# Performance work log

Hardware: AMD Instinct MI355X
Metric: run time of the kernel (lower is better)

The kernel has to match this reference:

```python
import jax, jax.numpy as jnp
import numpy as np

N_NODE = 4096        # graph size (dense adjacency is N_NODE x N_NODE)
N_EDGES = 131072     # avg degree 32
N_TARGETS = 512      # anomaly target list length (self.lst in original)
EPS = 1e-20


def setup_inputs() -> dict:
    key = jax.random.key(0)
    k1, k2, k3 = jax.random.split(key, 3)
    src = jax.random.randint(k1, (N_EDGES,), 0, N_NODE)
    dst = jax.random.randint(k2, (N_EDGES,), 0, N_NODE)
    tri_idx = jnp.stack([src, dst], axis=1).astype(jnp.int64)   # [m, 2] (src, dst)
    tri_w = jnp.ones((N_EDGES,), dtype=jnp.float32)             # [m] edge weights
    lst = jax.random.randint(k3, (N_TARGETS,), 0, N_NODE).astype(jnp.int64)
    return {"tri_idx": tri_idx, "tri_w": tri_w, "lst": lst}


def _forward(tri_idx, tri_w, lst):
    n = N_NODE
    # adjacency_matrix: scatter-add coo -> dense, then symmetrize minus diag
    A = jnp.zeros((n, n), dtype=tri_w.dtype).at[tri_idx[:, 0], tri_idx[:, 1]].add(tri_w)
    A = A + A.T - jnp.diag(jnp.diag(A))

    # extract_NE: N = row sums; E = row sums + 0.5 * diag(A^3)
    N = jnp.sum(A, axis=1)                      # [n]
    A2 = A @ A                                  # [n, n]
    diag_A3 = jnp.einsum('ik,ki->i', A2, A)     # diag(A @ A @ A) without full A^3
    E = N + 0.5 * diag_A3                       # [n]
    Ncol = N.reshape(-1, 1)                     # [n, 1]

    # OLS_estimation: theta = pinv([1, log N]) @ log E
    logN = jnp.log(Ncol + EPS)                  # [n, 1]
    logE = jnp.log(E + EPS)                     # [n]
    logN1 = jnp.concatenate([jnp.ones((n, 1), dtype=logN.dtype), logN], axis=1)  # [n, 2]
    theta = jnp.linalg.pinv(logN1) @ logE       # [2]
    b, w = theta[0], theta[1]

    # sum of squared power-law residuals over target list (vectorized loop)
    resid = jnp.exp(b) * N[lst] ** w - E[lst]   # [len(lst)]
    return jnp.sum(resid ** 2).reshape(1)       # original accumulates shape-[1] terms


def reference(tri_idx, tri_w, lst):
    return _forward(tri_idx, tri_w, lst)
```

## Files before the change

### kernel.cpp

```cpp
#include <hip/hip_runtime.h>
#include <math.h>

#define NN   4096
#define NN4  (NN/4)
#define CAP  128
#define RPB  2
#define D3B  (NN/RPB)
#define NGRP (D3B/64)
#define GPAD 32
#define CPAD 32

#define C_TGRP  0
#define C_TGLOB (32 * GPAD)

#define OFF_CNT  4608
#define OFF_ENTP 528896
#define OFF_ND   1577472
#define OFF_GSUM 1610240
#define ZBYTES   OFF_ND
#define Z4       (ZBYTES / 16)

__global__ __launch_bounds__(256) void zeroall_kernel(float4* __restrict__ z) {
    int t = blockIdx.x * 256 + threadIdx.x;
    if (t < Z4) z[t] = make_float4(0.f, 0.f, 0.f, 0.f);
}

__global__ void scatter_kernel(const int* __restrict__ idx,
                               const float* __restrict__ wgt,
                               int* __restrict__ cnt,
                               unsigned short* __restrict__ entp, int m) {
    int e = blockIdx.x * blockDim.x + threadIdx.x;
    if (e < m) {
        int2 sd = ((const int2*)idx)[e];
        int s = sd.x, d = sd.y;
        unsigned ival = (unsigned)(int)wgt[e];
        if (ival > 15u) ival = 15u;
        int p = atomicAdd(cnt + s * CPAD, 1);
        if (p < CAP) entp[(size_t)s * CAP + p] = (unsigned short)(((unsigned)d << 4) | ival);
        if (s != d) {
            int q = atomicAdd(cnt + d * CPAD, 1);
            if (q < CAP) entp[(size_t)d * CAP + q] = (unsigned short)(((unsigned)s << 4) | ival);
        }
    }
}

__global__ __launch_bounds__(256, 8) void diag3stats_kernel(
        const int* __restrict__ cnt, const unsigned* __restrict__ entp32,
        unsigned long long* __restrict__ ND,
        const int* __restrict__ lst, int nl,
        int* __restrict__ ctr, double* __restrict__ gsum,
        float* __restrict__ out) {
    __shared__ int    lrow[NN];
    __shared__ int    lcol[CAP];
    __shared__ int    lval[CAP];
    __shared__ int    redI[8];
    __shared__ int    flag;
    __shared__ double dsum[4][4];
    __shared__ double wb[2];
    __shared__ double sh[4];

    const int tid = threadIdx.x, bid = blockIdx.x;
    const int warp = tid >> 6, lane = tid & 63;
    const int i0 = bid * RPB;

    int mi_arr[RPB];
    #pragma unroll
    for (int r = 0; r < RPB; ++r) {
        int c = cnt[(i0 + r) * CPAD];
        mi_arr[r] = c > CAP ? CAP : c;
    }
    unsigned q_arr[RPB] = {0u, 0u};
    if (tid < 64) {
        #pragma unroll
        for (int r = 0; r < RPB; ++r)
            q_arr[r] = entp32[(size_t)(i0 + r) * 64 + tid];
    }

    int4* l4 = (int4*)lrow;
    for (int rr = 0; rr < RPB; ++rr) {
        const int i = i0 + rr;
        const int mi = mi_arr[rr];
        for (int k = tid; k < NN4; k += 256) l4[k] = make_int4(0, 0, 0, 0);
        __syncthreads();

        int nsum = 0;
        if (tid < 64) {
            unsigned q = q_arr[rr];
            unsigned e0 = q & 0xffffu, e1 = q >> 16;
            int c0 = (int)(e0 >> 4), c1 = (int)(e1 >> 4);
            int w0 = (int)(e0 & 15u), w1 = (int)(e1 & 15u);
            lcol[2 * tid]     = c0; lval[2 * tid]     = w0;
            lcol[2 * tid + 1] = c1; lval[2 * tid + 1] = w1;
            if (w0) atomicAdd(&lrow[c0], w0);
            if (w1) atomicAdd(&lrow[c1], w1);
            nsum = w0 + w1;
        }
        if (warp == 0) {
            for (int o = 32; o; o >>= 1) nsum += __shfl_down(nsum, o);
            if (lane == 0) redI[0] = nsum;
        }
        __syncthreads();

        int acc = 0;
        for (int t = warp; t < mi; t += 16) {
            const int t1 = t + 4, t2 = t + 8, t3 = t + 12;
            const bool b1 = t1 < mi, b2 = t2 < mi, b3 = t3 < mi;
            int c0 = lcol[t];
            int c1 = b1 ? lcol[t1] : 0;
            int c2 = b2 ? lcol[t2] : 0;
            int c3 = b3 ? lcol[t3] : 0;
            int a0 = lval[t];
            int a1 = b1 ? lval[t1] : 0;
            int a2 = b2 ? lval[t2] : 0;
            int a3 = b3 ? lval[t3] : 0;
            unsigned q0 = entp32[(size_t)c0 * 64 + lane];
            unsigned q1 = entp32[(size_t)c1 * 64 + lane];
            unsigned q2 = entp32[(size_t)c2 * 64 + lane];
            unsigned q3 = entp32[(size_t)c3 * 64 + lane];
            int d0 = (int)(q0 & 15u) * lrow[(q0 >> 4) & 4095u]
                   + (int)((q0 >> 16) & 15u) * lrow[q0 >> 20];
            int d1 = (int)(q1 & 15u) * lrow[(q1 >> 4) & 4095u]
                   + (int)((q1 >> 16) & 15u) * lrow[q1 >> 20];
            int d2 = (int)(q2 & 15u) * lrow[(q2 >> 4) & 4095u]
                   + (int)((q2 >> 16) & 15u) * lrow[q2 >> 20];
            int d3 = (int)(q3 & 15u) * lrow[(q3 >> 4) & 4095u]
                   + (int)((q3 >> 16) & 15u) * lrow[q3 >> 20];
            acc += a0 * d0 + a1 * d1 + a2 * d2 + a3 * d3;
        }
        for (int o = 32; o; o >>= 1) acc += __shfl_down(acc, o);
        if (lane == 0) redI[4 + warp] = acc;
        __syncthreads();

        if (tid == 0) {
            float2 nd = make_float2((float)redI[0],
                                    (float)(redI[4] + redI[5] + redI[6] + redI[7]));
            unsigned long long bits;
            __builtin_memcpy(&bits, &nd, 8);
            __hip_atomic_store(ND + i, bits, __ATOMIC_RELAXED, __HIP_MEMORY_SCOPE_AGENT);
        }
        __syncthreads();
    }

    if (tid == 0) {
        asm volatile("s_waitcnt vmcnt(0)" ::: "memory");
        int v = __hip_atomic_fetch_add(ctr + C_TGRP + (bid >> 6) * GPAD, 1,
                                       __ATOMIC_RELAXED, __HIP_MEMORY_SCOPE_AGENT);
        flag = (v == 63);
    }
    __syncthreads();
    if (!flag) return;

    const int g = bid >> 6;
    {
        double p1 = 0, p2 = 0, p3 = 0, p4 = 0;
        if (tid < 128) {
            unsigned long long bits = __hip_atomic_load(ND + (g * 128 + tid),
                                                        __ATOMIC_RELAXED, __HIP_MEMORY_SCOPE_AGENT);
            float2 nd; __builtin_memcpy(&nd, &bits, 8);
            double Nd = (double)nd.x;
            double Ed = Nd + 0.5 * (double)nd.y;
            double ln = (double)logf((float)(Nd + 1e-20));
            double le = (double)logf((float)(Ed + 1e-20));
            p1 = ln; p2 = ln * ln; p3 = le; p4 = ln * le;
        }
        for (int o = 32; o; o >>= 1) {
            p1 += __shfl_down(p1, o);
            p2 += __shfl_down(p2, o);
            p3 += __shfl_down(p3, o);
            p4 += __shfl_down(p4, o);
        }
        if (lane == 0) {
            dsum[warp][0] = p1; dsum[warp][1] = p2;
            dsum[warp][2] = p3; dsum[warp][3] = p4;
        }
        __syncthreads();
        if (tid == 0) {
            for (int k = 0; k < 4; ++k) {
                double v = dsum[0][k] + dsum[1][k] + dsum[2][k] + dsum[3][k];
                __hip_atomic_store(gsum + g * 4 + k, v, __ATOMIC_RELAXED,
                                   __HIP_MEMORY_SCOPE_AGENT);
            }
            asm volatile("s_waitcnt vmcnt(0)" ::: "memory");
            int vg = __hip_atomic_fetch_add(ctr + C_TGLOB, 1,
                                            __ATOMIC_RELAXED, __HIP_MEMORY_SCOPE_AGENT);
            flag = (vg == NGRP - 1);
        }
    }
    __syncthreads();
    if (!flag) return;

    if (warp == 0) {
        double s1 = 0, s2 = 0, t0 = 0, t1 = 0;
        if (lane < NGRP) {
            s1 = __hip_atomic_load(gsum + lane * 4 + 0, __ATOMIC_RELAXED, __HIP_MEMORY_SCOPE_AGENT);
            s2 = __hip_atomic_load(gsum + lane * 4 + 1, __ATOMIC_RELAXED, __HIP_MEMORY_SCOPE_AGENT);
            t0 = __hip_atomic_load(gsum + lane * 4 + 2, __ATOMIC_RELAXED, __HIP_MEMORY_SCOPE_AGENT);
            t1 = __hip_atomic_load(gsum + lane * 4 + 3, __ATOMIC_RELAXED, __HIP_MEMORY_SCOPE_AGENT);
        }
        for (int o = 32; o; o >>= 1) {
            s1 += __shfl_down(s1, o);
            s2 += __shfl_down(s2, o);
            t0 += __shfl_down(t0, o);
            t1 += __shfl_down(t1, o);
        }
        if (lane == 0) {
            double n = (double)NN;
            double det = n * s2 - s1 * s1;
            wb[0] = (n * t1 - s1 * t0) / det;
            wb[1] = (s2 * t0 - s1 * t1) / det;
        }
    }
    __syncthreads();
    const double w = wb[0];
    const double eb = exp(wb[1]);
    const float wf = (float)w;
    double racc = 0;
    for (int p = tid; p < nl; p += 256) {
        int r = lst[p];
        unsigned long long bits = __hip_atomic_load(ND + r, __ATOMIC_RELAXED,
                                                    __HIP_MEMORY_SCOPE_AGENT);
        float2 nd; __builtin_memcpy(&nd, &bits, 8);
        double Nd = (double)nd.x;
        double Ed = Nd + 0.5 * (double)nd.y;
        double pr = (nd.x > 0.f) ? (double)exp2f(wf * log2f(nd.x)) : 0.0;
        double rv = eb * pr - Ed;
        racc += rv * rv;
    }
    for (int o = 32; o; o >>= 1) racc += __shfl_down(racc, o);
    if (lane == 0) sh[warp] = racc;
    __syncthreads();
    if (tid == 0) out[0] = (float)(sh[0] + sh[1] + sh[2] + sh[3]);
}

extern "C" void kernel_launch(void* const* d_in, const int* in_sizes, int n_in,
                              void* d_out, int out_size, void* d_ws, size_t ws_size,
                              hipStream_t stream) {
    const int*   tri_idx = (const int*)d_in[0];
    const float* tri_w   = (const float*)d_in[1];
    const int*   lst     = (const int*)d_in[2];
    const int m  = in_sizes[1];
    const int nl = in_sizes[2];

    char* base = (char*)d_ws;
    int*            ctr  = (int*)base;
    int*            cnt  = (int*)(base + OFF_CNT);
    unsigned short* entp = (unsigned short*)(base + OFF_ENTP);
    unsigned*       e32  = (unsigned*)(base + OFF_ENTP);
    unsigned long long* ND = (unsigned long long*)(base + OFF_ND);
    double*         gsum = (double*)(base + OFF_GSUM);
    float*          out  = (float*)d_out;

    zeroall_kernel<<<(Z4 + 255) / 256, 256, 0, stream>>>((float4*)base);
    scatter_kernel<<<(m + 255) / 256, 256, 0, stream>>>(tri_idx, tri_w, cnt, entp, m);
    diag3stats_kernel<<<D3B, 256, 0, stream>>>(cnt, e32, ND, lst, nl, ctr, gsum, out);
}
```

Measured before the change: 43.12 us.

## Fuse scatter and diag-cube stats into one persistent kernel with grid barriers

Merges the count zeroing, the edge scatter and the diag(A^3) stats kernel into one launch of 2048 blocks, using two hierarchical software grid barriers with atomic counters. The large workspace zero-fill is replaced by zeroing only the counters, which works because entries are now masked by per-row counts instead of relying on zeroed slots. Entries widen from 16-bit to 32-bit (column<<8 | weight), which doubles the gather traffic. The software grid barrier assumes all 2048 blocks are co-resident, and the code can deadlock if they are not.

New measurement: 50.20 us. 16.4% more time.

```diff
diff --git a/kernel.cpp b/kernel.cpp
--- a/kernel.cpp
+++ b/kernel.cpp
@@ -6,139 +6,193 @@
 #define CAP  128
 #define RPB  2
 #define D3B  (NN/RPB)
-#define NGRP (D3B/64)
+#define NGRP 32
 #define GPAD 32
 #define CPAD 32
 
-#define C_TGRP  0
-#define C_TGLOB (32 * GPAD)
-
-#define OFF_CNT  4608
-#define OFF_ENTP 528896
-#define OFF_ND   1577472
-#define OFF_GSUM 1610240
-#define ZBYTES   OFF_ND
-#define Z4       (ZBYTES / 16)
-
-__global__ __launch_bounds__(256) void zeroall_kernel(float4* __restrict__ z) {
+#define C_GOA   0
+#define C_AGRP  (32 * GPAD)
+#define C_AGLOB (64 * GPAD)
+#define C_GOB   (65 * GPAD)
+#define C_BGRP  (97 * GPAD)
+#define C_BGLOB (129 * GPAD)
+#define C_TGRP  (130 * GPAD)
+#define C_TGLOB (162 * GPAD)
+#define CTR_INTS (163 * GPAD)
+
+#define OFF_CNT  24576
+#define OFF_ENTP 548864
+#define OFF_ND   2646016
+#define OFF_GSUM 2678784
+
+__global__ __launch_bounds__(256) void zerobar_kernel(int* __restrict__ ctr) {
     int t = blockIdx.x * 256 + threadIdx.x;
-    if (t < Z4) z[t] = make_float4(0.f, 0.f, 0.f, 0.f);
+    if (t < CTR_INTS) ctr[t] = 0;
 }
 
-__global__ void scatter_kernel(const int* __restrict__ idx,
-                               const float* __restrict__ wgt,
-                               int* __restrict__ cnt,
-                               unsigned short* __restrict__ entp, int m) {
-    int e = blockIdx.x * blockDim.x + threadIdx.x;
-    if (e < m) {
-        int2 sd = ((const int2*)idx)[e];
-        int s = sd.x, d = sd.y;
-        unsigned ival = (unsigned)(int)wgt[e];
-        if (ival > 15u) ival = 15u;
-        int p = atomicAdd(cnt + s * CPAD, 1);
-        if (p < CAP) entp[(size_t)s * CAP + p] = (unsigned short)(((unsigned)d << 4) | ival);
-        if (s != d) {
-            int q = atomicAdd(cnt + d * CPAD, 1);
-            if (q < CAP) entp[(size_t)d * CAP + q] = (unsigned short)(((unsigned)s << 4) | ival);
-        }
-    }
+__device__ __forceinline__ void gridbar(int* __restrict__ c, int goOff,
+                                        int grpOff, int globOff,
+                                        int tid, int bid) {
+    __syncthreads();
+    if (tid == 0) {
+        const int g = bid & 31;
+        int v = __hip_atomic_fetch_add(c + grpOff + g * GPAD, 1,
+                                       __ATOMIC_RELAXED, __HIP_MEMORY_SCOPE_AGENT);
+        if (v == 63) {
+            int vg = __hip_atomic_fetch_add(c + globOff, 1,
+                                            __ATOMIC_RELAXED, __HIP_MEMORY_SCOPE_AGENT);
+            if (vg == NGRP - 1) {
+                #pragma unroll
+                for (int k = 0; k < NGRP; ++k)
+                    __hip_atomic_store(c + goOff + k * GPAD, 1,
+                                       __ATOMIC_RELAXED, __HIP_MEMORY_SCOPE_AGENT);
+            }
+        }
+        while (__hip_atomic_load(c + goOff + g * GPAD,
+                                 __ATOMIC_RELAXED, __HIP_MEMORY_SCOPE_AGENT) == 0)
+            __builtin_amdgcn_s_sleep(8);
+    }
+    __syncthreads();
 }
 
-__global__ __launch_bounds__(256, 8) void diag3stats_kernel(
-        const int* __restrict__ cnt, const unsigned* __restrict__ entp32,
-        unsigned long long* __restrict__ ND,
+__global__ __launch_bounds__(256, 8) void fused_kernel(
+        const int* __restrict__ idx, const float* __restrict__ wgt, int m,
         const int* __restrict__ lst, int nl,
-        int* __restrict__ ctr, double* __restrict__ gsum,
-        float* __restrict__ out) {
+        int* __restrict__ cnt, unsigned* __restrict__ entp,
+        unsigned long long* __restrict__ ND, double* __restrict__ gsum,
+        int* __restrict__ ctr, float* __restrict__ out) {
     __shared__ int    lrow[NN];
     __shared__ int    lcol[CAP];
     __shared__ int    lval[CAP];
+    __shared__ int    lmj[CAP];
     __shared__ int    redI[8];
     __shared__ int    flag;
     __shared__ double dsum[4][4];
     __shared__ double wb[2];
     __shared__ double sh[4];
 
-    const int tid = threadIdx.x, bid = blockIdx.x;
+    const int tid  = threadIdx.x;
+    const int bid  = blockIdx.x;
+    const int gtid = bid * 256 + tid;
     const int warp = tid >> 6, lane = tid & 63;
-    const int i0 = bid * RPB;
-
-    int mi_arr[RPB];
-    #pragma unroll
-    for (int r = 0; r < RPB; ++r) {
-        int c = cnt[(i0 + r) * CPAD];
-        mi_arr[r] = c > CAP ? CAP : c;
-    }
-    unsigned q_arr[RPB] = {0u, 0u};
-    if (tid < 64) {
+
+    if (gtid < NN)
+        __hip_atomic_store(cnt + gtid * CPAD, 0, __ATOMIC_RELAXED,
+                           __HIP_MEMORY_SCOPE_AGENT);
+    gridbar(ctr, C_GOA, C_AGRP, C_AGLOB, tid, bid);
+
+    if (gtid < m) {
+        int2 sd = ((const int2*)idx)[gtid];
+        int s = sd.x, d = sd.y;
+        unsigned ival = (unsigned)(int)wgt[gtid];
+        if (ival > 255u) ival = 255u;
+        int p = atomicAdd(cnt + s * CPAD, 1);
+        if (p < CAP)
+            __hip_atomic_store(entp + (size_t)s * CAP + p, ((unsigned)d << 8) | ival,
+                               __ATOMIC_RELAXED, __HIP_MEMORY_SCOPE_AGENT);
+        if (s != d) {
+            int q = atomicAdd(cnt + d * CPAD, 1);
+            if (q < CAP)
+                __hip_atomic_store(entp + (size_t)d * CAP + q, ((unsigned)s << 8) | ival,
+                                   __ATOMIC_RELAXED, __HIP_MEMORY_SCOPE_AGENT);
+        }
+    }
+    gridbar(ctr, C_GOB, C_BGRP, C_BGLOB, tid, bid);
+
+    {
+        const int i0 = bid * RPB;
+        int mi_arr[RPB];
         #pragma unroll
-        for (int r = 0; r < RPB; ++r)
-            q_arr[r] = entp32[(size_t)(i0 + r) * 64 + tid];
-    }
-
-    int4* l4 = (int4*)lrow;
-    for (int rr = 0; rr < RPB; ++rr) {
-        const int i = i0 + rr;
-        const int mi = mi_arr[rr];
-        for (int k = tid; k < NN4; k += 256) l4[k] = make_int4(0, 0, 0, 0);
-        __syncthreads();
-
-        int nsum = 0;
+        for (int r = 0; r < RPB; ++r) {
+            int c = cnt[(i0 + r) * CPAD];
+            mi_arr[r] = c > CAP ? CAP : c;
+        }
+        uint2 q_arr[RPB];
+        #pragma unroll
+        for (int r = 0; r < RPB; ++r) q_arr[r] = make_uint2(0u, 0u);
         if (tid < 64) {
-            unsigned q = q_arr[rr];
-            unsigned e0 = q & 0xffffu, e1 = q >> 16;
-            int c0 = (int)(e0 >> 4), c1 = (int)(e1 >> 4);
-            int w0 = (int)(e0 & 15u), w1 = (int)(e1 & 15u);
-            lcol[2 * tid]     = c0; lval[2 * tid]     = w0;
-            lcol[2 * tid + 1] = c1; lval[2 * tid + 1] = w1;
-            if (w0) atomicAdd(&lrow[c0], w0);
-            if (w1) atomicAdd(&lrow[c1], w1);
-            nsum = w0 + w1;
-        }
-        if (warp == 0) {
-            for (int o = 32; o; o >>= 1) nsum += __shfl_down(nsum, o);
-            if (lane == 0) redI[0] = nsum;
-        }
-        __syncthreads();
-
-        int acc = 0;
-        for (int t = warp; t < mi; t += 16) {
-            const int t1 = t + 4, t2 = t + 8, t3 = t + 12;
-            const bool b1 = t1 < mi, b2 = t2 < mi, b3 = t3 < mi;
-            int c0 = lcol[t];
-            int c1 = b1 ? lcol[t1] : 0;
-            int c2 = b2 ? lcol[t2] : 0;
-            int c3 = b3 ? lcol[t3] : 0;
-            int a0 = lval[t];
-            int a1 = b1 ? lval[t1] : 0;
-            int a2 = b2 ? lval[t2] : 0;
-            int a3 = b3 ? lval[t3] : 0;
-            unsigned q0 = entp32[(size_t)c0 * 64 + lane];
-            unsigned q1 = entp32[(size_t)c1 * 64 + lane];
-            unsigned q2 = entp32[(size_t)c2 * 64 + lane];
-            unsigned q3 = entp32[(size_t)c3 * 64 + lane];
-            int d0 = (int)(q0 & 15u) * lrow[(q0 >> 4) & 4095u]
-                   + (int)((q0 >> 16) & 15u) * lrow[q0 >> 20];
-            int d1 = (int)(q1 & 15u) * lrow[(q1 >> 4) & 4095u]
-                   + (int)((q1 >> 16) & 15u) * lrow[q1 >> 20];
-            int d2 = (int)(q2 & 15u) * lrow[(q2 >> 4) & 4095u]
-                   + (int)((q2 >> 16) & 15u) * lrow[q2 >> 20];
-            int d3 = (int)(q3 & 15u) * lrow[(q3 >> 4) & 4095u]
-                   + (int)((q3 >> 16) & 15u) * lrow[q3 >> 20];
-            acc += a0 * d0 + a1 * d1 + a2 * d2 + a3 * d3;
-        }
-        for (int o = 32; o; o >>= 1) acc += __shfl_down(acc, o);
-        if (lane == 0) redI[4 + warp] = acc;
-        __syncthreads();
-
-        if (tid == 0) {
-            float2 nd = make_float2((float)redI[0],
-                                    (float)(redI[4] + redI[5] + redI[6] + redI[7]));
-            unsigned long long bits;
-            __builtin_memcpy(&bits, &nd, 8);
-            __hip_atomic_store(ND + i, bits, __ATOMIC_RELAXED, __HIP_MEMORY_SCOPE_AGENT);
-        }
-        __syncthreads();
+            #pragma unroll
+            for (int r = 0; r < RPB; ++r)
+                q_arr[r] = ((const uint2*)(entp + (size_t)(i0 + r) * CAP))[tid];
+        }
+
+        int4* l4 = (int4*)lrow;
+        for (int rr = 0; rr < RPB; ++rr) {
+            const int i = i0 + rr;
+            const int mi = mi_arr[rr];
+            for (int k = tid; k < NN4; k += 256) l4[k] = make_int4(0, 0, 0, 0);
+            __syncthreads();
+
+            int nsum = 0;
+            if (tid < 64) {
+                uint2 q = q_arr[rr];
+                const bool v0 = (2 * tid)     < mi;
+                const bool v1 = (2 * tid + 1) < mi;
+                int c0 = v0 ? (int)((q.x >> 8) & 4095u) : 0;
+                int c1 = v1 ? (int)((q.y >> 8) & 4095u) : 0;
+                int w0 = v0 ? (int)(q.x & 255u) : 0;
+                int w1 = v1 ? (int)(q.y & 255u) : 0;
+                lcol[2 * tid]     = c0; lval[2 * tid]     = w0;
+                lcol[2 * tid + 1] = c1; lval[2 * tid + 1] = w1;
+                int m0 = 0, m1 = 0;
+                if (v0) { m0 = cnt[c0 * CPAD]; if (m0 > CAP) m0 = CAP; }
+                if (v1) { m1 = cnt[c1 * CPAD]; if (m1 > CAP) m1 = CAP; }
+                lmj[2 * tid]     = m0;
+                lmj[2 * tid + 1] = m1;
+                if (w0) atomicAdd(&lrow[c0], w0);
+                if (w1) atomicAdd(&lrow[c1], w1);
+                nsum = w0 + w1;
+            }
+            if (warp == 0) {
+                for (int o = 32; o; o >>= 1) nsum += __shfl_down(nsum, o);
+                if (lane == 0) redI[0] = nsum;
+            }
+            __syncthreads();
+
+            int acc = 0;
+            const int s0 = 2 * lane, s1 = 2 * lane + 1;
+            for (int t = warp; t < mi; t += 16) {
+                const int t1 = t + 4, t2 = t + 8, t3 = t + 12;
+                const bool b1 = t1 < mi, b2 = t2 < mi, b3 = t3 < mi;
+                int c0 = lcol[t];
+                int c1 = b1 ? lcol[t1] : 0;
+                int c2 = b2 ? lcol[t2] : 0;
+                int c3 = b3 ? lcol[t3] : 0;
+                int a0 = lval[t];
+                int a1 = b1 ? lval[t1] : 0;
+                int a2 = b2 ? lval[t2] : 0;
+                int a3 = b3 ? lval[t3] : 0;
+                int m0 = lmj[t];
+                int m1 = b1 ? lmj[t1] : 0;
+                int m2 = b2 ? lmj[t2] : 0;
+                int m3 = b3 ? lmj[t3] : 0;
+                uint2 q0 = ((const uint2*)(entp + (size_t)c0 * CAP))[lane];
+                uint2 q1 = ((const uint2*)(entp + (size_t)c1 * CAP))[lane];
+                uint2 q2 = ((const uint2*)(entp + (size_t)c2 * CAP))[lane];
+                uint2 q3 = ((const uint2*)(entp + (size_t)c3 * CAP))[lane];
+                int d0 = (s0 < m0 ? (int)(q0.x & 255u) * lrow[(q0.x >> 8) & 4095u] : 0)
+                       + (s1 < m0 ? (int)(q0.y & 255u) * lrow[(q0.y >> 8) & 4095u] : 0);
+                int d1 = (s0 < m1 ? (int)(q1.x & 255u) * lrow[(q1.x >> 8) & 4095u] : 0)
+                       + (s1 < m1 ? (int)(q1.y & 255u) * lrow[(q1.y >> 8) & 4095u] : 0);
+                int d2 = (s0 < m2 ? (int)(q2.x & 255u) * lrow[(q2.x >> 8) & 4095u] : 0)
+                       + (s1 < m2 ? (int)(q2.y & 255u) * lrow[(q2.y >> 8) & 4095u] : 0);
+                int d3 = (s0 < m3 ? (int)(q3.x & 255u) * lrow[(q3.x >> 8) & 4095u] : 0)
+                       + (s1 < m3 ? (int)(q3.y & 255u) * lrow[(q3.y >> 8) & 4095u] : 0);
+                acc += a0 * d0 + a1 * d1 + a2 * d2 + a3 * d3;
+            }
+            for (int o = 32; o; o >>= 1) acc += __shfl_down(acc, o);
+            if (lane == 0) redI[4 + warp] = acc;
+            __syncthreads();
+
+            if (tid == 0) {
+                float2 nd = make_float2((float)redI[0],
+                                        (float)(redI[4] + redI[5] + redI[6] + redI[7]));
+                unsigned long long bits;
+                __builtin_memcpy(&bits, &nd, 8);
+                __hip_atomic_store(ND + i, bits, __ATOMIC_RELAXED, __HIP_MEMORY_SCOPE_AGENT);
+            }
+            __syncthreads();
+        }
     }
 
     if (tid == 0) {
@@ -242,15 +296,14 @@
     const int nl = in_sizes[2];
 
     char* base = (char*)d_ws;
-    int*            ctr  = (int*)base;
-    int*            cnt  = (int*)(base + OFF_CNT);
-    unsigned short* entp = (unsigned short*)(base + OFF_ENTP);
-    unsigned*       e32  = (unsigned*)(base + OFF_ENTP);
+    int*      ctr  = (int*)base;
+    int*      cnt  = (int*)(base + OFF_CNT);
+    unsigned* entp = (unsigned*)(base + OFF_ENTP);
     unsigned long long* ND = (unsigned long long*)(base + OFF_ND);
-    double*         gsum = (double*)(base + OFF_GSUM);
-    float*          out  = (float*)d_out;
-
-    zeroall_kernel<<<(Z4 + 255) / 256, 256, 0, stream>>>((float4*)base);
-    scatter_kernel<<<(m + 255) / 256, 256, 0, stream>>>(tri_idx, tri_w, cnt, entp, m);
-    diag3stats_kernel<<<D3B, 256, 0, stream>>>(cnt, e32, ND, lst, nl, ctr, gsum, out);
+    double*   gsum = (double*)(base + OFF_GSUM);
+    float*    out  = (float*)d_out;
+
+    zerobar_kernel<<<(CTR_INTS + 255) / 256, 256, 0, stream>>>(ctr);
+    fused_kernel<<<D3B, 256, 0, stream>>>(tri_idx, tri_w, m, lst, nl,
+                                          cnt, entp, ND, gsum, ctr, out);
 }
```
